# Performance work log

Hardware: AMD Instinct MI355X
Metric: run time of the kernel (lower is better)

Reference implementation:

```python
import jax, jax.numpy as jnp
import numpy as np

H = 768
NH = 12
HD = H // NH  # 64


def setup_inputs() -> dict:
    key = jax.random.key(0)
    ks = jax.random.split(key, 12)
    B, SQ, SK = 8, 1024, 1024
    s = 1.0 / np.sqrt(H)
    return {
        "hidden_states": jax.random.normal(ks[0], (B, SQ, H), jnp.float32),
        "condition_embeddings": jax.random.normal(ks[1], (B, SK, H), jnp.float32),
        "condition_mask": jnp.ones((B, SK), jnp.float32),
        "Wq": jax.random.normal(ks[2], (H, H), jnp.float32) * s,
        "bq": jnp.zeros((H,), jnp.float32),
        "Wk": jax.random.normal(ks[3], (H, H), jnp.float32) * s,
        "bk": jnp.zeros((H,), jnp.float32),
        "Wv": jax.random.normal(ks[4], (H, H), jnp.float32) * s,
        "bv": jnp.zeros((H,), jnp.float32),
        "Wo": jax.random.normal(ks[5], (H, H), jnp.float32) * s,
        "bo": jnp.zeros((H,), jnp.float32),
        "ln_g": jnp.ones((H,), jnp.float32),
        "ln_b": jnp.zeros((H,), jnp.float32),
    }


def _heads(x):
    # [B, S, H] -> [B, NH, S, HD]
    B, S, _ = x.shape
    return x.reshape(B, S, NH, HD).transpose(0, 2, 1, 3)


def reference(hidden_states, condition_embeddings, condition_mask,
              Wq, bq, Wk, bk, Wv, bv, Wo, bo, ln_g, ln_b):
    q = _heads(hidden_states @ Wq.T + bq)            # [B,NH,SQ,HD]
    k = _heads(condition_embeddings @ Wk.T + bk)     # [B,NH,SK,HD]
    v = _heads(condition_embeddings @ Wv.T + bv)     # [B,NH,SK,HD]

    scores = jnp.einsum("bhqd,bhkd->bhqk", q, k) / np.sqrt(HD)
    ext_mask = (1.0 - condition_mask)[:, None, None, :] * -10000.0
    scores = scores + ext_mask
    probs = jax.nn.softmax(scores, axis=-1)          # dropout = identity (eval)

    ctx = jnp.einsum("bhqk,bhkd->bhqd", probs, v)    # [B,NH,SQ,HD]
    B, _, SQ, _ = ctx.shape
    ctx = ctx.transpose(0, 2, 1, 3).reshape(B, SQ, H)

    out = ctx @ Wo.T + bo
    x = hidden_states + out
    mu = jnp.mean(x, axis=-1, keepdims=True)
    var = jnp.var(x, axis=-1, keepdims=True)
    return (x - mu) / jnp.sqrt(var + 1e-5) * ln_g + ln_b
```

## Files before the change

kernel.cpp:

```cpp
#include <hip/hip_runtime.h>
#include <stdint.h>

#define B_ 8
#define S_ 1024
#define H_ 768
#define NH_ 12
#define HD_ 64
#define M_ (B_*S_)

typedef __attribute__((ext_vector_type(8))) short short8;
typedef __attribute__((ext_vector_type(4))) float floatx4;

#define MFMA16(a,b,c) __builtin_amdgcn_mfma_f32_16x16x32_bf16((a),(b),(c),0,0,0)

__device__ __forceinline__ ushort f2bf(float x){
    union { float f; unsigned u; } v; v.f = x;
    unsigned r = (v.u + 0x7fffu + ((v.u >> 16) & 1u)) >> 16;
    return (ushort)r;
}

__device__ __forceinline__ void async16(const ushort* g, ushort* l){
    __builtin_amdgcn_global_load_lds(
        (const __attribute__((address_space(1))) unsigned int*)g,
        (__attribute__((address_space(3))) unsigned int*)l, 16, 0, 0);
}

__global__ __launch_bounds__(256, 8) void cvt_all(
    const float* __restrict__ hs, const float* __restrict__ ce,
    const float* __restrict__ wq, const float* __restrict__ wk,
    const float* __restrict__ wv, const float* __restrict__ wo,
    ushort* __restrict__ hsb, ushort* __restrict__ ceb,
    ushort* __restrict__ wqb, ushort* __restrict__ wkb,
    ushort* __restrict__ wvb, ushort* __restrict__ wob)
{
    const int NA = M_*H_/4;
    const int NW = H_*H_/4;
    int i = blockIdx.x*256 + threadIdx.x;
    if (i >= 2*NA + 4*NW) return;
    const float* s; ushort* d; int off;
    if (i < NA)            { s = hs; d = hsb; off = i; }
    else if (i < 2*NA)     { s = ce; d = ceb; off = i - NA; }
    else {
        int j = i - 2*NA;
        int wsel = j / NW;
        off = j - wsel*NW;
        s = (wsel==0) ? wq : (wsel==1) ? wk : (wsel==2) ? wv : wo;
        d = (wsel==0) ? wqb : (wsel==1) ? wkb : (wsel==2) ? wvb : wob;
    }
    float4 f = ((const float4*)s)[off];
    ushort4 u;
    u.x = f2bf(f.x); u.y = f2bf(f.y); u.z = f2bf(f.z); u.w = f2bf(f.w);
    ((ushort4*)d)[off] = u;
}

__device__ __forceinline__ void gemm_body(
    const ushort* __restrict__ A, const ushort* __restrict__ Bw,
    const float* __restrict__ bias, ushort* __restrict__ obf,
    float* __restrict__ of32, const float* __restrict__ resid,
    int mode, int bx, int by)
{
    __shared__ ushort smem[16384];
    ushort* lA = smem;
    ushort* lB = smem + 8192;
    const int K = H_;
    int tid  = threadIdx.x;
    int lane = tid & 63, wave = tid >> 6;
    int m0 = bx * 128, n0 = by * 128;
    int wm = (wave >> 1) * 64, wn = (wave & 1) * 64;
    int fr = lane & 15, quad = lane >> 4, quad4 = quad*4;

    floatx4 acc[4][4];
    #pragma unroll
    for (int mt=0;mt<4;mt++)
        #pragma unroll
        for (int nt=0;nt<4;nt++)
            acc[mt][nt] = (floatx4){0.f,0.f,0.f,0.f};

    int row0 = tid >> 3;
    int csw  = ((tid & 7) ^ (row0 & 7)) * 8;
    const ushort* Ap[4]; const ushort* Bp[4];
    ushort* ldA_[4]; ushort* ldB_[4];
    #pragma unroll
    for (int j=0;j<4;j++){
        int row = row0 + 32*j;
        Ap[j] = A  + (size_t)(m0 + row) * K + csw;
        Bp[j] = Bw + (size_t)(n0 + row) * K + csw;
        ldA_[j] = lA + (tid + 256*j)*8;
        ldB_[j] = lB + (tid + 256*j)*8;
    }

    for (int k0 = 0; k0 < K; k0 += 64){
        #pragma unroll
        for (int j=0;j<4;j++) async16(Ap[j] + k0, ldA_[j]);
        #pragma unroll
        for (int j=0;j<4;j++) async16(Bp[j] + k0, ldB_[j]);
        __syncthreads();
        #pragma unroll
        for (int kk=0; kk<2; kk++){
            short8 af[4], bfr[4];
            #pragma unroll
            for (int t=0;t<4;t++){
                int ra = wm + t*16 + fr;
                int rb = wn + t*16 + fr;
                af[t]  = *(const short8*)&lA[ra*64 + (((kk*4+quad) ^ (ra&7))<<3)];
                bfr[t] = *(const short8*)&lB[rb*64 + (((kk*4+quad) ^ (rb&7))<<3)];
            }
            #pragma unroll
            for (int mt=0;mt<4;mt++)
                #pragma unroll
                for (int nt=0;nt<4;nt++)
                    acc[mt][nt] = MFMA16(af[mt], bfr[nt], acc[mt][nt]);
        }
        __syncthreads();
    }

    float bv_[4];
    #pragma unroll
    for (int nt=0;nt<4;nt++) bv_[nt] = bias[n0 + wn + nt*16 + fr];

    if (mode == 0){
        #pragma unroll
        for (int mt=0;mt<4;mt++){
            int rb = m0 + wm + mt*16 + quad4;
            #pragma unroll
            for (int nt=0;nt<4;nt++){
                int col = n0 + wn + nt*16 + fr;
                #pragma unroll
                for (int r=0;r<4;r++)
                    obf[(size_t)(rb + r)*H_ + col] = f2bf(acc[mt][nt][r] + bv_[nt]);
            }
        }
    } else if (mode == 1){
        int bb = m0 >> 10, q0 = m0 & 1023;
        #pragma unroll
        for (int nh=0; nh<2; nh++){
            __syncthreads();
            if ((wave & 1) == nh){
                #pragma unroll
                for (int mt=0;mt<4;mt++){
                    int ql = wm + mt*16 + quad4;
                    #pragma unroll
                    for (int nt=0;nt<4;nt++){
                        int dl = nt*16 + fr;
                        ushort4 u;
                        u.x = f2bf(acc[mt][nt][0] + bv_[nt]);
                        u.y = f2bf(acc[mt][nt][1] + bv_[nt]);
                        u.z = f2bf(acc[mt][nt][2] + bv_[nt]);
                        u.w = f2bf(acc[mt][nt][3] + bv_[nt]);
                        *(ushort4*)&smem[dl*136 + ql] = u;
                    }
                }
            }
            __syncthreads();
            int head = by*2 + nh;
            #pragma unroll
            for (int jj=0;jj<4;jj++){
                int mI = tid + 256*jj;
                int d  = mI >> 4;
                int qc = (mI & 15) * 8;
                short8 v = *(const short8*)&smem[d*136 + qc];
                *(short8*)&obf[((size_t)((bb*NH_ + head)*HD_ + d))*S_ + q0 + qc] = v;
            }
        }
    } else {
        #pragma unroll
        for (int mt=0;mt<4;mt++){
            int rb = m0 + wm + mt*16 + quad4;
            #pragma unroll
            for (int nt=0;nt<4;nt++){
                int col = n0 + wn + nt*16 + fr;
                #pragma unroll
                for (int r=0;r<4;r++){
                    size_t idx = (size_t)(rb + r)*H_ + col;
                    of32[idx] = acc[mt][nt][r] + bv_[nt] + resid[idx];
                }
            }
        }
    }
}

__global__ __launch_bounds__(256, 3) void gemm_qkv(
    const ushort* __restrict__ hsb, const ushort* __restrict__ ceb,
    const ushort* __restrict__ wqb, const ushort* __restrict__ wkb,
    const ushort* __restrict__ wvb,
    const float* __restrict__ bq, const float* __restrict__ bk,
    const float* __restrict__ bv,
    ushort* __restrict__ Qb, ushort* __restrict__ Kb, ushort* __restrict__ Vtb)
{
    int z = blockIdx.z;
    const ushort* A  = (z==0) ? hsb : ceb;
    const ushort* Bw = (z==0) ? wqb : (z==1) ? wkb : wvb;
    const float* bias = (z==0) ? bq : (z==1) ? bk : bv;
    ushort* obf = (z==0) ? Qb : (z==1) ? Kb : Vtb;
    gemm_body(A, Bw, bias, obf, nullptr, nullptr, (z==2) ? 1 : 0,
              blockIdx.x, blockIdx.y);
}

__global__ __launch_bounds__(256, 3) void gemm_o(
    const ushort* __restrict__ ctxb, const ushort* __restrict__ wob,
    const float* __restrict__ bo, const float* __restrict__ hs,
    float* __restrict__ proj)
{
    gemm_body(ctxb, wob, bo, nullptr, proj, hs, 2, blockIdx.x, blockIdx.y);
}

__global__ __launch_bounds__(256, 3) void attn(
    const ushort* __restrict__ Q, const ushort* __restrict__ Kc,
    const ushort* __restrict__ Vt, const float* __restrict__ mask,
    ushort* __restrict__ ctx)
{
    __shared__ ushort lK[64*64];
    __shared__ ushort lV[64*64];
    __shared__ ushort lP[4][32*72];
    __shared__ float  lmask[S_];
    __shared__ float  linv[4][32];

    const float SC = 0.125f * 1.44269504f;

    int bid = blockIdx.x;
    int qt = bid & 7;
    int h  = (bid >> 3) % NH_;
    int b  = bid / (8*NH_);

    int tid  = threadIdx.x;
    int lane = tid & 63, w = tid >> 6;
    int fr = lane & 15, quad = lane >> 4;
    int quad4 = quad*4, sw = fr & 7;

    for (int i = tid; i < S_; i += 256)
        lmask[i] = (1.0f - mask[b*S_ + i]) * -14426.95f;

    short8 qf[2][2];
    #pragma unroll
    for (int nq=0;nq<2;nq++){
        const ushort* Qp = Q + (size_t)(b*S_ + qt*128 + w*32 + nq*16 + fr)*H_ + h*HD_ + quad*8;
        qf[nq][0] = *(const short8*)(Qp);
        qf[nq][1] = *(const short8*)(Qp + 32);
    }

    floatx4 O[2][4];
    #pragma unroll
    for (int mt=0;mt<2;mt++)
        #pragma unroll
        for (int nt=0;nt<4;nt++)
            O[mt][nt] = (floatx4){0.f,0.f,0.f,0.f};
    float rs0 = 0.f, rs1 = 0.f;

    int n0 = tid,       r0 = n0 >> 3, c0 = (n0 & 7) ^ (r0 & 7);
    int n1 = 256 + tid, r1 = n1 >> 3, c1 = (n1 & 7) ^ (r1 & 7);
    const ushort* pK0 = Kc + (size_t)(b*S_ + r0)*H_ + h*HD_ + c0*8;
    const ushort* pK1 = Kc + (size_t)(b*S_ + r1)*H_ + h*HD_ + c1*8;
    const ushort* pV0 = Vt + ((size_t)(b*NH_ + h)*HD_ + r0)*S_ + c0*8;
    const ushort* pV1 = Vt + ((size_t)(b*NH_ + h)*HD_ + r1)*S_ + c1*8;
    ushort* dK0 = &lK[n0*8]; ushort* dK1 = &lK[n1*8];
    ushort* dV0 = &lV[n0*8]; ushort* dV1 = &lV[n1*8];

    ushort* lPw = &lP[w][0];

    for (int kt = 0; kt < 16; kt++){
        __syncthreads();
        async16(pK0, dK0); async16(pK1, dK1);
        async16(pV0, dV0); async16(pV1, dV1);
        pK0 += (size_t)64*H_; pK1 += (size_t)64*H_;
        pV0 += 64; pV1 += 64;
        __syncthreads();

        float4 mk4[4];
        #pragma unroll
        for (int mk=0;mk<4;mk++)
            mk4[mk] = *(const float4*)&lmask[kt*64 + mk*16 + quad4];

        short8 kf[4][2];
        #pragma unroll
        for (int mk=0;mk<4;mk++){
            int row = mk*16 + fr;
            kf[mk][0] = *(const short8*)&lK[row*64 + ((quad     ^ sw)<<3)];
            kf[mk][1] = *(const short8*)&lK[row*64 + (((4+quad) ^ sw)<<3)];
        }
        __builtin_amdgcn_s_setprio(1);
        floatx4 st[2][4];
        #pragma unroll
        for (int nq=0;nq<2;nq++)
            #pragma unroll
            for (int mk=0;mk<4;mk++){
                floatx4 a = (floatx4){0.f,0.f,0.f,0.f};
                a = MFMA16(kf[mk][0], qf[nq][0], a);
                a = MFMA16(kf[mk][1], qf[nq][1], a);
                st[nq][mk] = a;
            }
        __builtin_amdgcn_s_setprio(0);

        #pragma unroll
        for (int nq=0;nq<2;nq++){
            #pragma unroll
            for (int mk=0;mk<4;mk++){
                floatx4 s = st[nq][mk];
                #pragma unroll
                for (int r=0;r<4;r++)
                    s[r] = __builtin_amdgcn_exp2f(s[r]*SC + mk4[mk][r]);
                if (nq == 0) rs0 += (s[0]+s[1]) + (s[2]+s[3]);
                else         rs1 += (s[0]+s[1]) + (s[2]+s[3]);
                unsigned lo = __builtin_amdgcn_perm(__float_as_uint(s[1]), __float_as_uint(s[0]), 0x07060302u);
                unsigned hi = __builtin_amdgcn_perm(__float_as_uint(s[3]), __float_as_uint(s[2]), 0x07060302u);
                uint2 pk; pk.x = lo; pk.y = hi;
                *(uint2*)&lPw[(nq*16 + fr)*72 + mk*16 + quad4] = pk;
            }
        }

        short8 vf[4][2];
        #pragma unroll
        for (int nt=0;nt<4;nt++){
            int row = nt*16 + fr;
            vf[nt][0] = *(const short8*)&lV[row*64 + ((quad     ^ sw)<<3)];
            vf[nt][1] = *(const short8*)&lV[row*64 + (((4+quad) ^ sw)<<3)];
        }
        short8 pf[2][2];
        #pragma unroll
        for (int mt=0;mt<2;mt++){
            pf[mt][0] = *(const short8*)&lPw[(mt*16+fr)*72 + quad*8];
            pf[mt][1] = *(const short8*)&lPw[(mt*16+fr)*72 + 32 + quad*8];
        }
        __builtin_amdgcn_s_setprio(1);
        #pragma unroll
        for (int mt=0;mt<2;mt++)
            #pragma unroll
            for (int nt=0;nt<4;nt++){
                O[mt][nt] = MFMA16(pf[mt][0], vf[nt][0], O[mt][nt]);
                O[mt][nt] = MFMA16(pf[mt][1], vf[nt][1], O[mt][nt]);
            }
        __builtin_amdgcn_s_setprio(0);
    }

    rs0 += __shfl_xor(rs0, 16); rs0 += __shfl_xor(rs0, 32);
    rs1 += __shfl_xor(rs1, 16); rs1 += __shfl_xor(rs1, 32);
    if (lane < 16){
        linv[w][fr]      = 1.0f / rs0;
        linv[w][16 + fr] = 1.0f / rs1;
    }
    int tokbase = b*S_ + qt*128 + w*32;
    #pragma unroll
    for (int mt=0;mt<2;mt++){
        float4 iv = *(const float4*)&linv[w][mt*16 + quad4];
        #pragma unroll
        for (int nt=0;nt<4;nt++)
            #pragma unroll
            for (int r=0;r<4;r++){
                int tok = tokbase + mt*16 + quad4 + r;
                ctx[(size_t)tok*H_ + h*HD_ + nt*16 + fr] = f2bf(O[mt][nt][r] * (&iv.x)[r]);
            }
    }
}

__global__ __launch_bounds__(192, 4) void resid_ln(
    const float* __restrict__ x,
    const float* __restrict__ g, const float* __restrict__ be,
    float* __restrict__ out)
{
    int row = blockIdx.x;
    int tid = threadIdx.x;
    float4 v = ((const float4*)(x + (size_t)row*H_))[tid];
    float s  = (v.x + v.y) + (v.z + v.w);
    float s2 = (v.x*v.x + v.y*v.y) + (v.z*v.z + v.w*v.w);
    #pragma unroll
    for (int off=1; off<64; off<<=1){
        s  += __shfl_xor(s,  off);
        s2 += __shfl_xor(s2, off);
    }
    __shared__ float rs[3], rs2[3];
    if ((tid & 63) == 0){ rs[tid>>6] = s; rs2[tid>>6] = s2; }
    __syncthreads();
    s  = rs[0]+rs[1]+rs[2];
    s2 = rs2[0]+rs2[1]+rs2[2];
    float mu  = s * (1.f/H_);
    float var = s2*(1.f/H_) - mu*mu;
    float rinv = rsqrtf(var + 1e-5f);
    float4 gg = ((const float4*)g)[tid];
    float4 bb = ((const float4*)be)[tid];
    float4 o;
    o.x = (v.x-mu)*rinv*gg.x + bb.x;
    o.y = (v.y-mu)*rinv*gg.y + bb.y;
    o.z = (v.z-mu)*rinv*gg.z + bb.z;
    o.w = (v.w-mu)*rinv*gg.w + bb.w;
    ((float4*)(out + (size_t)row*H_))[tid] = o;
}

extern "C" void kernel_launch(void* const* d_in, const int* in_sizes, int n_in,
                              void* d_out, int out_size, void* d_ws, size_t ws_size,
                              hipStream_t stream)
{
    (void)in_sizes; (void)n_in; (void)out_size; (void)ws_size;
    const float* hs   = (const float*)d_in[0];
    const float* ce   = (const float*)d_in[1];
    const float* mask = (const float*)d_in[2];
    const float* Wq   = (const float*)d_in[3];
    const float* bq   = (const float*)d_in[4];
    const float* Wk   = (const float*)d_in[5];
    const float* bk   = (const float*)d_in[6];
    const float* Wv   = (const float*)d_in[7];
    const float* bv   = (const float*)d_in[8];
    const float* Wo   = (const float*)d_in[9];
    const float* bo   = (const float*)d_in[10];
    const float* lg   = (const float*)d_in[11];
    const float* lb   = (const float*)d_in[12];
    float* out = (float*)d_out;

    char* ws = (char*)d_ws;
    const size_t SZ_ACT = (size_t)M_*H_*2;
    const size_t SZ_W   = (size_t)H_*H_*2;
    ushort* hsb  = (ushort*)(ws);
    ushort* ceb  = (ushort*)(ws + SZ_ACT);
    ushort* wqb  = (ushort*)(ws + 2*SZ_ACT);
    ushort* wkb  = (ushort*)(ws + 2*SZ_ACT + 1*SZ_W);
    ushort* wvb  = (ushort*)(ws + 2*SZ_ACT + 2*SZ_W);
    ushort* wob  = (ushort*)(ws + 2*SZ_ACT + 3*SZ_W);
    ushort* Qb   = (ushort*)(ws + 2*SZ_ACT + 4*SZ_W);
    ushort* Kb   = (ushort*)(ws + 3*SZ_ACT + 4*SZ_W);
    ushort* Vtb  = (ushort*)(ws + 4*SZ_ACT + 4*SZ_W);
    ushort* ctxb = (ushort*)(ws + 5*SZ_ACT + 4*SZ_W);
    float*  proj = (float*)(ws);

    int ncvt = 2*(M_*H_/4) + 4*(H_*H_/4);
    cvt_all<<<dim3((ncvt+255)/256), dim3(256), 0, stream>>>(
        hs, ce, Wq, Wk, Wv, Wo, hsb, ceb, wqb, wkb, wvb, wob);

    gemm_qkv<<<dim3(M_/128, H_/128, 3), dim3(256), 0, stream>>>(
        hsb, ceb, wqb, wkb, wvb, bq, bk, bv, Qb, Kb, Vtb);

    attn<<<dim3(B_*NH_*8), dim3(256), 0, stream>>>(Qb, Kb, Vtb, mask, ctxb);

    gemm_o<<<dim3(M_/128, H_/128), dim3(256), 0, stream>>>(ctxb, wob, bo, hs, proj);

    resid_ln<<<dim3(M_), dim3(192), 0, stream>>>(proj, lg, lb, out);
}
```

Before: 226.7 us.

## Use 128x96 tiles for QKV GEMM and register-prefetch K/V tiles in attention

```diff
diff --git a/kernel.cpp b/kernel.cpp
--- a/kernel.cpp
+++ b/kernel.cpp
@@ -53,39 +53,45 @@
     ((ushort4*)d)[off] = u;
 }
 
+template<int BN, int MODE>
 __device__ __forceinline__ void gemm_body(
     const ushort* __restrict__ A, const ushort* __restrict__ Bw,
     const float* __restrict__ bias, ushort* __restrict__ obf,
     float* __restrict__ of32, const float* __restrict__ resid,
-    int mode, int bx, int by)
-{
-    __shared__ ushort smem[16384];
+    int bx, int by)
+{
+    constexpr int NT = BN/32;
+    __shared__ ushort smem[8192 + BN*64];
     ushort* lA = smem;
     ushort* lB = smem + 8192;
     const int K = H_;
     int tid  = threadIdx.x;
     int lane = tid & 63, wave = tid >> 6;
-    int m0 = bx * 128, n0 = by * 128;
-    int wm = (wave >> 1) * 64, wn = (wave & 1) * 64;
+    int m0 = bx * 128, n0 = by * BN;
+    int wm = (wave >> 1) * 64, wn = (wave & 1) * (BN/2);
     int fr = lane & 15, quad = lane >> 4, quad4 = quad*4;
 
-    floatx4 acc[4][4];
+    floatx4 acc[4][NT];
     #pragma unroll
     for (int mt=0;mt<4;mt++)
         #pragma unroll
-        for (int nt=0;nt<4;nt++)
+        for (int nt=0;nt<NT;nt++)
             acc[mt][nt] = (floatx4){0.f,0.f,0.f,0.f};
 
     int row0 = tid >> 3;
     int csw  = ((tid & 7) ^ (row0 & 7)) * 8;
-    const ushort* Ap[4]; const ushort* Bp[4];
-    ushort* ldA_[4]; ushort* ldB_[4];
+    const ushort* Ap[4]; const ushort* Bp[NT];
+    ushort* ldA_[4]; ushort* ldB_[NT];
     #pragma unroll
     for (int j=0;j<4;j++){
         int row = row0 + 32*j;
         Ap[j] = A  + (size_t)(m0 + row) * K + csw;
+        ldA_[j] = lA + (tid + 256*j)*8;
+    }
+    #pragma unroll
+    for (int j=0;j<NT;j++){
+        int row = row0 + 32*j;
         Bp[j] = Bw + (size_t)(n0 + row) * K + csw;
-        ldA_[j] = lA + (tid + 256*j)*8;
         ldB_[j] = lB + (tid + 256*j)*8;
     }
 
@@ -93,81 +99,79 @@
         #pragma unroll
         for (int j=0;j<4;j++) async16(Ap[j] + k0, ldA_[j]);
         #pragma unroll
-        for (int j=0;j<4;j++) async16(Bp[j] + k0, ldB_[j]);
+        for (int j=0;j<NT;j++) async16(Bp[j] + k0, ldB_[j]);
         __syncthreads();
         #pragma unroll
         for (int kk=0; kk<2; kk++){
-            short8 af[4], bfr[4];
+            short8 af[4], bfr[NT];
             #pragma unroll
             for (int t=0;t<4;t++){
                 int ra = wm + t*16 + fr;
+                af[t]  = *(const short8*)&lA[ra*64 + (((kk*4+quad) ^ (ra&7))<<3)];
+            }
+            #pragma unroll
+            for (int t=0;t<NT;t++){
                 int rb = wn + t*16 + fr;
-                af[t]  = *(const short8*)&lA[ra*64 + (((kk*4+quad) ^ (ra&7))<<3)];
                 bfr[t] = *(const short8*)&lB[rb*64 + (((kk*4+quad) ^ (rb&7))<<3)];
             }
             #pragma unroll
             for (int mt=0;mt<4;mt++)
                 #pragma unroll
-                for (int nt=0;nt<4;nt++)
+                for (int nt=0;nt<NT;nt++)
                     acc[mt][nt] = MFMA16(af[mt], bfr[nt], acc[mt][nt]);
         }
         __syncthreads();
     }
 
-    float bv_[4];
-    #pragma unroll
-    for (int nt=0;nt<4;nt++) bv_[nt] = bias[n0 + wn + nt*16 + fr];
-
-    if (mode == 0){
+    float bv_[NT];
+    #pragma unroll
+    for (int nt=0;nt<NT;nt++) bv_[nt] = bias[n0 + wn + nt*16 + fr];
+
+    if constexpr (MODE == 0){
         #pragma unroll
         for (int mt=0;mt<4;mt++){
             int rb = m0 + wm + mt*16 + quad4;
             #pragma unroll
-            for (int nt=0;nt<4;nt++){
+            for (int nt=0;nt<NT;nt++){
                 int col = n0 + wn + nt*16 + fr;
                 #pragma unroll
                 for (int r=0;r<4;r++)
                     obf[(size_t)(rb + r)*H_ + col] = f2bf(acc[mt][nt][r] + bv_[nt]);
             }
         }
-    } else if (mode == 1){
+    } else if constexpr (MODE == 1){
         int bb = m0 >> 10, q0 = m0 & 1023;
         #pragma unroll
-        for (int nh=0; nh<2; nh++){
-            __syncthreads();
-            if ((wave & 1) == nh){
-                #pragma unroll
-                for (int mt=0;mt<4;mt++){
-                    int ql = wm + mt*16 + quad4;
-                    #pragma unroll
-                    for (int nt=0;nt<4;nt++){
-                        int dl = nt*16 + fr;
-                        ushort4 u;
-                        u.x = f2bf(acc[mt][nt][0] + bv_[nt]);
-                        u.y = f2bf(acc[mt][nt][1] + bv_[nt]);
-                        u.z = f2bf(acc[mt][nt][2] + bv_[nt]);
-                        u.w = f2bf(acc[mt][nt][3] + bv_[nt]);
-                        *(ushort4*)&smem[dl*136 + ql] = u;
-                    }
-                }
-            }
-            __syncthreads();
-            int head = by*2 + nh;
-            #pragma unroll
-            for (int jj=0;jj<4;jj++){
-                int mI = tid + 256*jj;
-                int d  = mI >> 4;
-                int qc = (mI & 15) * 8;
-                short8 v = *(const short8*)&smem[d*136 + qc];
-                *(short8*)&obf[((size_t)((bb*NH_ + head)*HD_ + d))*S_ + q0 + qc] = v;
-            }
+        for (int mt=0;mt<4;mt++){
+            int ql = wm + mt*16 + quad4;
+            #pragma unroll
+            for (int nt=0;nt<NT;nt++){
+                int dl = wn + nt*16 + fr;
+                ushort4 u;
+                u.x = f2bf(acc[mt][nt][0] + bv_[nt]);
+                u.y = f2bf(acc[mt][nt][1] + bv_[nt]);
+                u.z = f2bf(acc[mt][nt][2] + bv_[nt]);
+                u.w = f2bf(acc[mt][nt][3] + bv_[nt]);
+                *(ushort4*)&smem[dl*136 + ql] = u;
+            }
+        }
+        __syncthreads();
+        #pragma unroll
+        for (int jj=0;jj<6;jj++){
+            int mI = tid + 256*jj;
+            int d  = mI >> 4;
+            int qc = (mI & 15) * 8;
+            short8 v = *(const short8*)&smem[d*136 + qc];
+            int gcol = by*96 + d;
+            int h = gcol >> 6, dd = gcol & 63;
+            *(short8*)&obf[((size_t)((bb*NH_ + h)*HD_ + dd))*S_ + q0 + qc] = v;
         }
     } else {
         #pragma unroll
         for (int mt=0;mt<4;mt++){
             int rb = m0 + wm + mt*16 + quad4;
             #pragma unroll
-            for (int nt=0;nt<4;nt++){
+            for (int nt=0;nt<NT;nt++){
                 int col = n0 + wn + nt*16 + fr;
                 #pragma unroll
                 for (int r=0;r<4;r++){
@@ -191,9 +195,10 @@
     const ushort* A  = (z==0) ? hsb : ceb;
     const ushort* Bw = (z==0) ? wqb : (z==1) ? wkb : wvb;
     const float* bias = (z==0) ? bq : (z==1) ? bk : bv;
-    ushort* obf = (z==0) ? Qb : (z==1) ? Kb : Vtb;
-    gemm_body(A, Bw, bias, obf, nullptr, nullptr, (z==2) ? 1 : 0,
-              blockIdx.x, blockIdx.y);
+    if (z == 2)
+        gemm_body<96,1>(A, Bw, bias, Vtb, nullptr, nullptr, blockIdx.x, blockIdx.y);
+    else
+        gemm_body<96,0>(A, Bw, bias, (z==0)?Qb:Kb, nullptr, nullptr, blockIdx.x, blockIdx.y);
 }
 
 __global__ __launch_bounds__(256, 3) void gemm_o(
@@ -201,7 +206,7 @@
     const float* __restrict__ bo, const float* __restrict__ hs,
     float* __restrict__ proj)
 {
-    gemm_body(ctxb, wob, bo, nullptr, proj, hs, 2, blockIdx.x, blockIdx.y);
+    gemm_body<128,2>(ctxb, wob, bo, nullptr, proj, hs, blockIdx.x, blockIdx.y);
 }
 
 __global__ __launch_bounds__(256, 3) void attn(
@@ -226,25 +231,6 @@
     int lane = tid & 63, w = tid >> 6;
     int fr = lane & 15, quad = lane >> 4;
     int quad4 = quad*4, sw = fr & 7;
-
-    for (int i = tid; i < S_; i += 256)
-        lmask[i] = (1.0f - mask[b*S_ + i]) * -14426.95f;
-
-    short8 qf[2][2];
-    #pragma unroll
-    for (int nq=0;nq<2;nq++){
-        const ushort* Qp = Q + (size_t)(b*S_ + qt*128 + w*32 + nq*16 + fr)*H_ + h*HD_ + quad*8;
-        qf[nq][0] = *(const short8*)(Qp);
-        qf[nq][1] = *(const short8*)(Qp + 32);
-    }
-
-    floatx4 O[2][4];
-    #pragma unroll
-    for (int mt=0;mt<2;mt++)
-        #pragma unroll
-        for (int nt=0;nt<4;nt++)
-            O[mt][nt] = (floatx4){0.f,0.f,0.f,0.f};
-    float rs0 = 0.f, rs1 = 0.f;
 
     int n0 = tid,       r0 = n0 >> 3, c0 = (n0 & 7) ^ (r0 & 7);
     int n1 = 256 + tid, r1 = n1 >> 3, c1 = (n1 & 7) ^ (r1 & 7);
@@ -255,15 +241,45 @@
     ushort* dK0 = &lK[n0*8]; ushort* dK1 = &lK[n1*8];
     ushort* dV0 = &lV[n0*8]; ushort* dV1 = &lV[n1*8];
 
+    float4 rK0 = *(const float4*)pK0;
+    float4 rK1 = *(const float4*)pK1;
+    float4 rV0 = *(const float4*)pV0;
+    float4 rV1 = *(const float4*)pV1;
+
+    for (int i = tid; i < S_; i += 256)
+        lmask[i] = (1.0f - mask[b*S_ + i]) * -14426.95f;
+
+    short8 qf[2][2];
+    #pragma unroll
+    for (int nq=0;nq<2;nq++){
+        const ushort* Qp = Q + (size_t)(b*S_ + qt*128 + w*32 + nq*16 + fr)*H_ + h*HD_ + quad*8;
+        qf[nq][0] = *(const short8*)(Qp);
+        qf[nq][1] = *(const short8*)(Qp + 32);
+    }
+
+    floatx4 O[2][4];
+    #pragma unroll
+    for (int mt=0;mt<2;mt++)
+        #pragma unroll
+        for (int nt=0;nt<4;nt++)
+            O[mt][nt] = (floatx4){0.f,0.f,0.f,0.f};
+    float rs0 = 0.f, rs1 = 0.f;
+
     ushort* lPw = &lP[w][0];
 
     for (int kt = 0; kt < 16; kt++){
         __syncthreads();
-        async16(pK0, dK0); async16(pK1, dK1);
-        async16(pV0, dV0); async16(pV1, dV1);
-        pK0 += (size_t)64*H_; pK1 += (size_t)64*H_;
-        pV0 += 64; pV1 += 64;
+        *(float4*)dK0 = rK0; *(float4*)dK1 = rK1;
+        *(float4*)dV0 = rV0; *(float4*)dV1 = rV1;
         __syncthreads();
+        if (kt < 15){
+            pK0 += (size_t)64*H_; pK1 += (size_t)64*H_;
+            pV0 += 64; pV1 += 64;
+            rK0 = *(const float4*)pK0;
+            rK1 = *(const float4*)pK1;
+            rV0 = *(const float4*)pV0;
+            rV1 = *(const float4*)pV1;
+        }
 
         float4 mk4[4];
         #pragma unroll
@@ -423,7 +439,7 @@
     cvt_all<<<dim3((ncvt+255)/256), dim3(256), 0, stream>>>(
         hs, ce, Wq, Wk, Wv, Wo, hsb, ceb, wqb, wkb, wvb, wob);
 
-    gemm_qkv<<<dim3(M_/128, H_/128, 3), dim3(256), 0, stream>>>(
+    gemm_qkv<<<dim3(M_/128, H_/96, 3), dim3(256), 0, stream>>>(
         hsb, ceb, wqb, wkb, wvb, bq, bk, bv, Qb, Kb, Vtb);
 
     attn<<<dim3(B_*NH_*8), dim3(256), 0, stream>>>(Qb, Kb, Vtb, mask, ctxb);
```

Measured after the change: 235.6 us. +3.9%, slower.
